# Performance work log

Measured on AMD Instinct MI355X. Metric: run time of the kernel, lower is better.

Reference implementation:

```python
import jax, jax.numpy as jnp
import numpy as np

B, T = 4096, 1024
IN, H, N, OUT = 1, 40, 40, 1  # input_size, hidden_size, nr_nodes, output_size
SLOPE = 0.01  # LeakyReLU negative slope (torch default)


def setup_inputs() -> dict:
    key = jax.random.key(0)
    ks = jax.random.split(key, 9)
    s = lambda fan_in: 1.0 / np.sqrt(fan_in)
    u = lambda k, shape, fan_in: jax.random.uniform(k, shape, jnp.float32, -s(fan_in), s(fan_in))
    return {
        "inputs": jax.random.normal(ks[0], (B, T), dtype=jnp.float32),
        # H2H: Linear(41->40), LeakyReLU, Linear(40->40)
        "h2h_w1": u(ks[1], (N, IN + H), IN + H),
        "h2h_b1": u(ks[2], (N,), IN + H),
        "h2h_w2": u(ks[3], (H, N), N),
        "h2h_b2": u(ks[4], (H,), N),
        # H2O: Linear(41->40), LeakyReLU, Linear(40->1)
        "h2o_w1": u(ks[5], (N, IN + H), IN + H),
        "h2o_b1": u(ks[6], (N,), IN + H),
        "h2o_w2": u(ks[7], (OUT, N), N),
        "h2o_b2": u(ks[8], (OUT,), N),
    }


def reference(inputs, h2h_w1, h2h_b1, h2h_w2, h2h_b2, h2o_w1, h2o_b1, h2o_w2, h2o_b2):
    def step(hidden, u_t):
        # combined: [B, 1+H]
        combined = jnp.concatenate([u_t[:, None], hidden], axis=1)
        a = jax.nn.leaky_relu(combined @ h2h_w1.T + h2h_b1, SLOPE)
        hidden_new = a @ h2h_w2.T + h2h_b2                      # [B, H]
        o = jax.nn.leaky_relu(combined @ h2o_w1.T + h2o_b1, SLOPE)
        out_t = (o @ h2o_w2.T + h2o_b2)[:, 0]                   # [B]
        return hidden_new, out_t

    hidden0 = jnp.zeros((inputs.shape[0], H), dtype=inputs.dtype)
    _, ys = jax.lax.scan(step, hidden0, inputs.T)  # ys: [T, B]
    return ys.T  # [B, T]
```

## Files before the change

kernel.cpp:

```cpp
#include <hip/hip_runtime.h>
#include <hip/hip_bf16.h>


#define B_SZ 4096
#define T_SZ 1024
#define HID  40

typedef unsigned short u16;
typedef unsigned int   u32;

__device__ __forceinline__ float bf2f(u16 v) {
  union { u32 u; float f; } c; c.u = ((u32)v) << 16; return c.f;
}

template <bool BF>
__device__ __forceinline__ float ldg(const void* p, long i) {
  if (BF) return bf2f(((const u16*)p)[i]);
  return ((const float*)p)[i];
}

__device__ __forceinline__ bool detect_bf16(const void* w) {
  const u16* p = (const u16*)w;
  bool bf = true;
  for (int i = 0; i < 64; ++i) {
    float f = bf2f(p[i]);
    if (!(fabsf(f) <= 0.2f)) bf = false;
  }
  return bf;
}

template <bool BF>
__global__ __launch_bounds__(128, 2)
void rnn_kernel(const void* __restrict__ inp,
                const void* __restrict__ h2h_w1, const void* __restrict__ h2h_b1,
                const void* __restrict__ h2h_w2, const void* __restrict__ h2h_b2,
                const void* __restrict__ h2o_w1, const void* __restrict__ h2o_b1,
                const void* __restrict__ h2o_w2, const void* __restrict__ h2o_b2,
                void* __restrict__ out) {
  __shared__ __align__(16) float sH[4][44];
  __shared__ __align__(16) float sA[4][84];

  if (detect_bf16(h2h_w1) != BF) return;

  const int tid  = threadIdx.x;
  const int lane = tid & 63;
  const int wv   = tid >> 6;
  const int el   = lane & 3;
  const int w    = wv * 16 + (lane >> 2);

  const int a0 = (wv == 0) ? 3 * w : 48 + 2 * (w - 16);
  const int nA = (wv == 0) ? 3 : 2;
  const int rB = (wv == 0) ? ((w < 8) ? 32 + w : ((w == 8) ? 40 : -1)) : 2 * (w - 16);

  float4 w4[4][10];
  float  wu[3] = {0, 0, 0}, ba[3] = {0, 0, 0}, bb[2] = {0, 0};
#pragma unroll
  for (int q = 0; q < 3; ++q) {
    if (q < nA) {
      const int  j  = a0 + q;
      const bool hh = (j < HID);
      const void* wb1 = hh ? h2h_w1 : h2o_w1;
      const long  jr  = hh ? j : (j - HID);
      wu[q] = ldg<BF>(wb1, jr * 41);
      ba[q] = ldg<BF>(hh ? h2h_b1 : h2o_b1, jr);
#pragma unroll
      for (int i = 0; i < 10; ++i) {
        w4[q][i].x = ldg<BF>(wb1, jr * 41 + 1 + 4 * i);
        w4[q][i].y = ldg<BF>(wb1, jr * 41 + 2 + 4 * i);
        w4[q][i].z = ldg<BF>(wb1, jr * 41 + 3 + 4 * i);
        w4[q][i].w = ldg<BF>(wb1, jr * 41 + 4 + 4 * i);
      }
    }
  }
  if (wv == 0) {
    if (rB >= 0) {
      const bool isout = (rB == 40);
      const void* wb2 = isout ? h2o_w2 : h2h_w2;
      const long  rr  = isout ? 0 : rB;
      bb[0] = isout ? ldg<BF>(h2o_b2, 0) : ldg<BF>(h2h_b2, rB);
#pragma unroll
      for (int i = 0; i < 10; ++i) {
        w4[3][i].x = ldg<BF>(wb2, rr * 40 + 4 * i);
        w4[3][i].y = ldg<BF>(wb2, rr * 40 + 4 * i + 1);
        w4[3][i].z = ldg<BF>(wb2, rr * 40 + 4 * i + 2);
        w4[3][i].w = ldg<BF>(wb2, rr * 40 + 4 * i + 3);
      }
    }
  } else {
#pragma unroll
    for (int q = 0; q < 2; ++q) {
      const long r = rB + q;
      bb[q] = ldg<BF>(h2h_b2, r);
#pragma unroll
      for (int i = 0; i < 10; ++i) {
        w4[2 + q][i].x = ldg<BF>(h2h_w2, r * 40 + 4 * i);
        w4[2 + q][i].y = ldg<BF>(h2h_w2, r * 40 + 4 * i + 1);
        w4[2 + q][i].z = ldg<BF>(h2h_w2, r * 40 + 4 * i + 2);
        w4[2 + q][i].w = ldg<BF>(h2h_w2, r * 40 + 4 * i + 3);
      }
    }
  }

  for (int i = tid; i < 4 * 44; i += 128) ((float*)sH)[i] = 0.f;
  __syncthreads();

  const int  b    = blockIdx.x * 4 + el;
  const long base = (long)b * T_SZ;
  float u_cur = ldg<BF>(inp, base);

  for (int t = 0; t < T_SZ; ++t) {
    const float u_nxt = (t + 1 < T_SZ) ? ldg<BF>(inp, base + t + 1) : 0.f;

    float4 hv[10];
    {
      const float4* hp = (const float4*)sH[el];
#pragma unroll
      for (int i = 0; i < 10; ++i) hv[i] = hp[i];
    }
#pragma unroll
    for (int q = 0; q < 3; ++q) {
      if (q < nA) {
        float a = fmaf(u_cur, wu[q], ba[q]);
#pragma unroll
        for (int i = 0; i < 10; ++i) {
          a = fmaf(hv[i].x, w4[q][i].x, a);
          a = fmaf(hv[i].y, w4[q][i].y, a);
          a = fmaf(hv[i].z, w4[q][i].z, a);
          a = fmaf(hv[i].w, w4[q][i].w, a);
        }
        sA[el][a0 + q] = fmaxf(a, 0.01f * a);
      }
    }
    __syncthreads();

    if (wv == 1) {
      float4 av[10];
      {
        const float4* ap = (const float4*)sA[el];
#pragma unroll
        for (int i = 0; i < 10; ++i) av[i] = ap[i];
      }
#pragma unroll
      for (int q = 0; q < 2; ++q) {
        float a2 = bb[q];
#pragma unroll
        for (int i = 0; i < 10; ++i) {
          a2 = fmaf(av[i].x, w4[2 + q][i].x, a2);
          a2 = fmaf(av[i].y, w4[2 + q][i].y, a2);
          a2 = fmaf(av[i].z, w4[2 + q][i].z, a2);
          a2 = fmaf(av[i].w, w4[2 + q][i].w, a2);
        }
        sH[el][rB + q] = a2;
      }
    } else if (rB >= 0) {
      const float4* ap = (const float4*)(&sA[el][(rB == 40) ? 40 : 0]);
      float a2 = bb[0];
#pragma unroll
      for (int i = 0; i < 10; ++i) {
        const float4 a4 = ap[i];
        a2 = fmaf(a4.x, w4[3][i].x, a2);
        a2 = fmaf(a4.y, w4[3][i].y, a2);
        a2 = fmaf(a4.z, w4[3][i].z, a2);
        a2 = fmaf(a4.w, w4[3][i].w, a2);
      }
      if (rB < HID) {
        sH[el][rB] = a2;
      } else {
        if (BF) ((__hip_bfloat16*)out)[base + t] = __float2bfloat16(a2);
        else    ((float*)out)[base + t] = a2;
      }
    }
    __syncthreads();

    u_cur = u_nxt;
  }
}

extern "C" void kernel_launch(void* const* d_in, const int* in_sizes, int n_in,
                              void* d_out, int out_size, void* d_ws, size_t ws_size,
                              hipStream_t stream) {
  (void)in_sizes; (void)n_in; (void)out_size; (void)d_ws; (void)ws_size;
  rnn_kernel<false><<<dim3(B_SZ / 4), dim3(128), 0, stream>>>(
      d_in[0], d_in[1], d_in[2], d_in[3], d_in[4],
      d_in[5], d_in[6], d_in[7], d_in[8], d_out);
  rnn_kernel<true><<<dim3(B_SZ / 4), dim3(128), 0, stream>>>(
      d_in[0], d_in[1], d_in[2], d_in[3], d_in[4],
      d_in[5], d_in[6], d_in[7], d_in[8], d_out);
}
```

Measured before the change: 877.3 us.

## Split each dot product across lane pairs with DPP reduction to shorten serial chains

Reassigns work so each output neuron's 40-element dot product is split into two 20-element halves computed by adjacent lanes, combined with a DPP quad-perm swap. Each thread now owns 5 layer-1 rows and up to 3 layer-2 rows instead of 3/2 rows of full length. Both waves share the layer-2 work evenly, which removes the earlier imbalance. The aim is to shorten the per-timestep dependent FMA chain on this latency-bound recurrence. In exchange it adds cross-lane ops, and the loads of the 4-batch hidden state in LDS become more spread out.

After: 904.2 us. 1.03x slower.

```diff
diff --git a/kernel.cpp b/kernel.cpp
--- a/kernel.cpp
+++ b/kernel.cpp
@@ -17,6 +17,16 @@
 __device__ __forceinline__ float ldg(const void* p, long i) {
   if (BF) return bf2f(((const u16*)p)[i]);
   return ((const float*)p)[i];
+}
+
+template <bool BF>
+__device__ __forceinline__ float4 ldg4(const void* p, long i) {
+  float4 r;
+  r.x = ldg<BF>(p, i + 0);
+  r.y = ldg<BF>(p, i + 1);
+  r.z = ldg<BF>(p, i + 2);
+  r.w = ldg<BF>(p, i + 3);
+  return r;
 }
 
 __device__ __forceinline__ bool detect_bf16(const void* w) {
@@ -27,6 +37,11 @@
     if (!(fabsf(f) <= 0.2f)) bf = false;
   }
   return bf;
+}
+
+__device__ __forceinline__ float pair_other(float x) {
+  return __int_as_float(__builtin_amdgcn_update_dpp(
+      0, __float_as_int(x), 0xB1, 0xF, 0xF, true));
 }
 
 template <bool BF>
@@ -37,137 +52,135 @@
                 const void* __restrict__ h2o_w1, const void* __restrict__ h2o_b1,
                 const void* __restrict__ h2o_w2, const void* __restrict__ h2o_b2,
                 void* __restrict__ out) {
-  __shared__ __align__(16) float sH[4][44];
-  __shared__ __align__(16) float sA[4][84];
+  __shared__ __align__(16) float sH[4][40];
+  __shared__ __align__(16) float sA[4][88];
 
   if (detect_bf16(h2h_w1) != BF) return;
 
   const int tid  = threadIdx.x;
   const int lane = tid & 63;
   const int wv   = tid >> 6;
-  const int el   = lane & 3;
-  const int w    = wv * 16 + (lane >> 2);
-
-  const int a0 = (wv == 0) ? 3 * w : 48 + 2 * (w - 16);
-  const int nA = (wv == 0) ? 3 : 2;
-  const int rB = (wv == 0) ? ((w < 8) ? 32 + w : ((w == 8) ? 40 : -1)) : 2 * (w - 16);
-
-  float4 w4[4][10];
-  float  wu[3] = {0, 0, 0}, ba[3] = {0, 0, 0}, bb[2] = {0, 0};
-#pragma unroll
-  for (int q = 0; q < 3; ++q) {
-    if (q < nA) {
-      const int  j  = a0 + q;
-      const bool hh = (j < HID);
-      const void* wb1 = hh ? h2h_w1 : h2o_w1;
-      const long  jr  = hh ? j : (j - HID);
-      wu[q] = ldg<BF>(wb1, jr * 41);
-      ba[q] = ldg<BF>(hh ? h2h_b1 : h2o_b1, jr);
-#pragma unroll
-      for (int i = 0; i < 10; ++i) {
-        w4[q][i].x = ldg<BF>(wb1, jr * 41 + 1 + 4 * i);
-        w4[q][i].y = ldg<BF>(wb1, jr * 41 + 2 + 4 * i);
-        w4[q][i].z = ldg<BF>(wb1, jr * 41 + 3 + 4 * i);
-        w4[q][i].w = ldg<BF>(wb1, jr * 41 + 4 + 4 * i);
-      }
-    }
-  }
-  if (wv == 0) {
-    if (rB >= 0) {
-      const bool isout = (rB == 40);
-      const void* wb2 = isout ? h2o_w2 : h2h_w2;
-      const long  rr  = isout ? 0 : rB;
-      bb[0] = isout ? ldg<BF>(h2o_b2, 0) : ldg<BF>(h2h_b2, rB);
-#pragma unroll
-      for (int i = 0; i < 10; ++i) {
-        w4[3][i].x = ldg<BF>(wb2, rr * 40 + 4 * i);
-        w4[3][i].y = ldg<BF>(wb2, rr * 40 + 4 * i + 1);
-        w4[3][i].z = ldg<BF>(wb2, rr * 40 + 4 * i + 2);
-        w4[3][i].w = ldg<BF>(wb2, rr * 40 + 4 * i + 3);
-      }
-    }
-  } else {
-#pragma unroll
-    for (int q = 0; q < 2; ++q) {
-      const long r = rB + q;
-      bb[q] = ldg<BF>(h2h_b2, r);
-#pragma unroll
-      for (int i = 0; i < 10; ++i) {
-        w4[2 + q][i].x = ldg<BF>(h2h_w2, r * 40 + 4 * i);
-        w4[2 + q][i].y = ldg<BF>(h2h_w2, r * 40 + 4 * i + 1);
-        w4[2 + q][i].z = ldg<BF>(h2h_w2, r * 40 + 4 * i + 2);
-        w4[2 + q][i].w = ldg<BF>(h2h_w2, r * 40 + 4 * i + 3);
-      }
-    }
-  }
-
-  for (int i = tid; i < 4 * 44; i += 128) ((float*)sH)[i] = 0.f;
+  const int el   = (lane >> 4) & 3;
+  const int kh   = lane & 1;
+  const int wp   = (lane >> 1) & 7;
+  const int w    = wv * 8 + wp;
+  const int koff = kh * 20;
+
+  float4 wA[5][5];
+  float  wu[5], ba[5];
+#pragma unroll
+  for (int q = 0; q < 5; ++q) {
+    const int  j  = 5 * w + q;
+    const bool hh = (j < HID);
+    const void* w1p = hh ? h2h_w1 : h2o_w1;
+    const long  jr  = hh ? j : (j - HID);
+    wu[q] = (kh == 0) ? ldg<BF>(w1p, jr * 41) : 0.f;
+    ba[q] = (kh == 0) ? ldg<BF>(hh ? h2h_b1 : h2o_b1, jr) : 0.f;
+#pragma unroll
+    for (int i = 0; i < 5; ++i)
+      wA[q][i] = ldg4<BF>(w1p, jr * 41 + 1 + koff + 4 * i);
+  }
+
+  const int r2 = (w < 8) ? (32 + w) : ((w == 8) ? 40 : -1);
+  float4 wB[3][5];
+  float  bb[3] = {0.f, 0.f, 0.f};
+#pragma unroll
+  for (int q = 0; q < 2; ++q) {
+    const long r = w + 16 * q;
+    bb[q] = (kh == 0) ? ldg<BF>(h2h_b2, r) : 0.f;
+#pragma unroll
+    for (int i = 0; i < 5; ++i)
+      wB[q][i] = ldg4<BF>(h2h_w2, r * 40 + koff + 4 * i);
+  }
+  if (r2 == 40) {
+    bb[2] = (kh == 0) ? ldg<BF>(h2o_b2, 0) : 0.f;
+#pragma unroll
+    for (int i = 0; i < 5; ++i)
+      wB[2][i] = ldg4<BF>(h2o_w2, koff + 4 * i);
+  } else if (r2 >= 0) {
+    bb[2] = (kh == 0) ? ldg<BF>(h2h_b2, r2) : 0.f;
+#pragma unroll
+    for (int i = 0; i < 5; ++i)
+      wB[2][i] = ldg4<BF>(h2h_w2, (long)r2 * 40 + koff + 4 * i);
+  }
+
+  for (int i = tid; i < 4 * HID; i += 128) ((float*)sH)[i] = 0.f;
   __syncthreads();
 
   const int  b    = blockIdx.x * 4 + el;
   const long base = (long)b * T_SZ;
   float u_cur = ldg<BF>(inp, base);
 
+  const float4* hp  = (const float4*)(&sH[el][koff]);
+  const float4* ap  = (const float4*)(&sA[el][koff]);
+  const float4* op  = (const float4*)(&sA[el][40 + koff]);
+  float* sAw = &sA[el][5 * w];
+  float* sHw = &sH[el][w];
+
   for (int t = 0; t < T_SZ; ++t) {
     const float u_nxt = (t + 1 < T_SZ) ? ldg<BF>(inp, base + t + 1) : 0.f;
 
-    float4 hv[10];
-    {
-      const float4* hp = (const float4*)sH[el];
-#pragma unroll
-      for (int i = 0; i < 10; ++i) hv[i] = hp[i];
-    }
-#pragma unroll
-    for (int q = 0; q < 3; ++q) {
-      if (q < nA) {
-        float a = fmaf(u_cur, wu[q], ba[q]);
-#pragma unroll
-        for (int i = 0; i < 10; ++i) {
-          a = fmaf(hv[i].x, w4[q][i].x, a);
-          a = fmaf(hv[i].y, w4[q][i].y, a);
-          a = fmaf(hv[i].z, w4[q][i].z, a);
-          a = fmaf(hv[i].w, w4[q][i].w, a);
-        }
-        sA[el][a0 + q] = fmaxf(a, 0.01f * a);
+    float4 hv[5];
+#pragma unroll
+    for (int i = 0; i < 5; ++i) hv[i] = hp[i];
+#pragma unroll
+    for (int q = 0; q < 5; ++q) {
+      float a = fmaf(u_cur, wu[q], ba[q]);
+#pragma unroll
+      for (int i = 0; i < 5; ++i) {
+        a = fmaf(hv[i].x, wA[q][i].x, a);
+        a = fmaf(hv[i].y, wA[q][i].y, a);
+        a = fmaf(hv[i].z, wA[q][i].z, a);
+        a = fmaf(hv[i].w, wA[q][i].w, a);
       }
+      const float s   = a + pair_other(a);
+      const float act = fmaxf(s, 0.01f * s);
+      if (kh == 0) sAw[q] = act;
     }
     __syncthreads();
 
-    if (wv == 1) {
-      float4 av[10];
-      {
-        const float4* ap = (const float4*)sA[el];
-#pragma unroll
-        for (int i = 0; i < 10; ++i) av[i] = ap[i];
+    float4 av[5];
+#pragma unroll
+    for (int i = 0; i < 5; ++i) av[i] = ap[i];
+#pragma unroll
+    for (int q = 0; q < 2; ++q) {
+      float s = bb[q];
+#pragma unroll
+      for (int i = 0; i < 5; ++i) {
+        s = fmaf(av[i].x, wB[q][i].x, s);
+        s = fmaf(av[i].y, wB[q][i].y, s);
+        s = fmaf(av[i].z, wB[q][i].z, s);
+        s = fmaf(av[i].w, wB[q][i].w, s);
       }
-#pragma unroll
-      for (int q = 0; q < 2; ++q) {
-        float a2 = bb[q];
-#pragma unroll
-        for (int i = 0; i < 10; ++i) {
-          a2 = fmaf(av[i].x, w4[2 + q][i].x, a2);
-          a2 = fmaf(av[i].y, w4[2 + q][i].y, a2);
-          a2 = fmaf(av[i].z, w4[2 + q][i].z, a2);
-          a2 = fmaf(av[i].w, w4[2 + q][i].w, a2);
+      const float v = s + pair_other(s);
+      if (kh == 0) sHw[16 * q] = v;
+    }
+    if (r2 >= 0) {
+      float s = bb[2];
+      if (r2 == 40) {
+#pragma unroll
+        for (int i = 0; i < 5; ++i) {
+          const float4 o4 = op[i];
+          s = fmaf(o4.x, wB[2][i].x, s);
+          s = fmaf(o4.y, wB[2][i].y, s);
+          s = fmaf(o4.z, wB[2][i].z, s);
+          s = fmaf(o4.w, wB[2][i].w, s);
         }
-        sH[el][rB + q] = a2;
-      }
-    } else if (rB >= 0) {
-      const float4* ap = (const float4*)(&sA[el][(rB == 40) ? 40 : 0]);
-      float a2 = bb[0];
-#pragma unroll
-      for (int i = 0; i < 10; ++i) {
-        const float4 a4 = ap[i];
-        a2 = fmaf(a4.x, w4[3][i].x, a2);
-        a2 = fmaf(a4.y, w4[3][i].y, a2);
-        a2 = fmaf(a4.z, w4[3][i].z, a2);
-        a2 = fmaf(a4.w, w4[3][i].w, a2);
-      }
-      if (rB < HID) {
-        sH[el][rB] = a2;
+        const float v = s + pair_other(s);
+        if (kh == 0) {
+          if (BF) ((__hip_bfloat16*)out)[base + t] = __float2bfloat16(v);
+          else    ((float*)out)[base + t] = v;
+        }
       } else {
-        if (BF) ((__hip_bfloat16*)out)[base + t] = __float2bfloat16(a2);
-        else    ((float*)out)[base + t] = a2;
+#pragma unroll
+        for (int i = 0; i < 5; ++i) {
+          s = fmaf(av[i].x, wB[2][i].x, s);
+          s = fmaf(av[i].y, wB[2][i].y, s);
+          s = fmaf(av[i].z, wB[2][i].z, s);
+          s = fmaf(av[i].w, wB[2][i].w, s);
+        }
+        const float v = s + pair_other(s);
+        if (kh == 0) sH[el][r2] = v;
       }
     }
     __syncthreads();
```
